# Kernel optimization log

Hardware: AMD Instinct MI355X
Metric: run time of the kernel (lower is better)

Reference implementation:

```python
import jax, jax.numpy as jnp
import numpy as np

TOPN = 1000
MIN_SCORE = 0.05
NMS_THR = 0.5
MAX_OBJ = 100
B, A, C = 8, 100000, 80


def setup_inputs():
    key = jax.random.key(0)
    k1, k2, k3, k4 = jax.random.split(key, 4)
    cls_heads = jax.random.uniform(k1, (B, A, C), dtype=jnp.float32)  # sigmoid-like class scores
    reg_heads = (jax.random.normal(k2, (B, A, 4), dtype=jnp.float32) * 0.1)  # small tx,ty,tw,th
    ctr = jax.random.uniform(k3, (B, A, 2), minval=32.0, maxval=768.0)
    wh = jax.random.uniform(k4, (B, A, 2), minval=16.0, maxval=128.0)
    batch_anchors = jnp.concatenate([ctr - 0.5 * wh, ctr + 0.5 * wh], axis=-1)
    return {"cls_heads": cls_heads, "reg_heads": reg_heads, "batch_anchors": batch_anchors}


def _decode(reg, anchors):
    # snap tx,ty,tw,th to x1y1x2y2; original casts to int (truncation toward zero)
    awh = anchors[..., 2:4] - anchors[..., 0:2]
    actr = anchors[..., 0:2] + 0.5 * awh
    pwh = jnp.exp(reg[..., 2:4]) * awh
    pctr = reg[..., 0:2] * awh + actr
    boxes = jnp.concatenate([pctr - 0.5 * pwh, pctr + 0.5 * pwh], axis=-1)
    return jnp.trunc(boxes)  # matches torch .int() truncation, kept float


def _per_image(scores, classes, boxes):
    # score-threshold filter + descending sort + topn, done as masked top_k (fixed shapes)
    masked = jnp.where(scores > MIN_SCORE, scores, -jnp.inf)
    top_s, idx = jax.lax.top_k(masked, TOPN)
    valid = top_s > MIN_SCORE
    top_c = classes[idx].astype(jnp.float32)
    top_b = boxes[idx]  # [TOPN,4]

    # pairwise IoU (greedy python_nms math)
    wh = top_b[:, 2:4] - top_b[:, 0:2]
    area = jnp.clip(wh[:, 0] * wh[:, 1], 1e-4)  # clamp(min=0.0001)
    tl = jnp.maximum(top_b[:, None, 0:2], top_b[None, :, 0:2])
    br = jnp.minimum(top_b[:, None, 2:4], top_b[None, :, 2:4])
    sz = jnp.clip(br - tl, 0.0)
    inter = sz[..., 0] * sz[..., 1]
    union = jnp.clip(area[:, None] + area[None, :] - inter, 1e-4)
    iou = inter / union  # [TOPN,TOPN]

    ar = jnp.arange(TOPN)

    def body(i, supp):
        # box i, if not already suppressed, suppresses later boxes with iou >= thr
        return supp | ((~supp[i]) & (iou[i] >= NMS_THR) & (ar > i))

    supp = jax.lax.fori_loop(0, TOPN, body, ~valid)
    kept = (~supp) & valid

    # compact first MAX_OBJ kept detections (score order preserved); pad with -1 / zeros
    rank = jnp.cumsum(kept) - 1
    slot = jnp.where(kept & (rank < MAX_OBJ), rank, MAX_OBJ)  # dump slot MAX_OBJ
    out_s = jnp.full((MAX_OBJ + 1,), -1.0, jnp.float32).at[slot].set(jnp.where(kept, top_s, -1.0))[:MAX_OBJ]
    out_c = jnp.full((MAX_OBJ + 1,), -1.0, jnp.float32).at[slot].set(jnp.where(kept, top_c, -1.0))[:MAX_OBJ]
    out_b = jnp.zeros((MAX_OBJ + 1, 4), jnp.float32).at[slot].set(jnp.where(kept[:, None], top_b, 0.0))[:MAX_OBJ]
    return out_s, out_c, out_b


def reference(cls_heads, reg_heads, batch_anchors):
    scores = jnp.max(cls_heads, axis=2)        # [B,A]
    classes = jnp.argmax(cls_heads, axis=2)    # [B,A] int
    boxes = _decode(reg_heads, batch_anchors)  # [B,A,4]
    return jax.vmap(_per_image)(scores, classes, boxes)
```

## Files before the change

kernel.cpp:

```cpp
#include <hip/hip_runtime.h>
#include <cstdint>

#define NB 8
#define NA 100000
#define NC 80
#define TOPN 1000
#define MAXOBJ 100
#define NREG 64
#define REGCAP 256
#define CTRSTRIDE 32
#define SORTN 2048
#define MIN_SCORE 0.05f
#define NMS_THR 0.5f

__global__ __launch_bounds__(256) void k_scores(const float* __restrict__ cls,
                                                unsigned int* __restrict__ keys,
                                                int* __restrict__ clsid,
                                                unsigned long long* __restrict__ cand,
                                                unsigned int* __restrict__ n_cand) {
    const int b = blockIdx.y;
    const int t = threadIdx.x;
    const int lane = t & 63;
    const int sub = lane & 3;
    const int a = blockIdx.x * 64 + (t >> 2);
    const bool valid = (a < NA);
    const int aa = valid ? a : (NA - 1);

    const float4* p = (const float4*)(cls + ((size_t)b * NA + aa) * NC);

    float vm = -1e30f; int vi = 0x7FFFFFFF;
#pragma unroll
    for (int s = 0; s < 5; ++s) {
        float4 v = p[sub + s * 4];
        int c0 = (sub + s * 4) * 4;
        if (v.x > vm) { vm = v.x; vi = c0; }
        if (v.y > vm) { vm = v.y; vi = c0 + 1; }
        if (v.z > vm) { vm = v.z; vi = c0 + 2; }
        if (v.w > vm) { vm = v.w; vi = c0 + 3; }
    }
#pragma unroll
    for (int d = 1; d < 4; d <<= 1) {
        float ovm = __shfl_xor(vm, d);
        int ovi = __shfl_xor(vi, d);
        if (ovm > vm || (ovm == vm && ovi < vi)) { vm = ovm; vi = ovi; }
    }

    unsigned int key = (vm > MIN_SCORE) ? __float_as_uint(vm) : 0u;
    if (valid && sub == 0) {
        size_t o = (size_t)b * NA + a;
        keys[o] = key;
        clsid[o] = vi;
    }

    const unsigned int T0 = __float_as_uint(0.999f);
    bool w = valid && (sub == 0) && (key >= T0);
    unsigned long long m = __ballot(w);
    if (m) {
        const int r = blockIdx.x & (NREG - 1);
        unsigned int* ctr = n_cand + (size_t)((b << 6) | r) * CTRSTRIDE;
        unsigned long long* creg = cand + ((size_t)((b << 6) | r)) * REGCAP;
        int leader = (int)__builtin_ctzll(m);
        unsigned int bs = 0;
        if (lane == leader) bs = atomicAdd(ctr, (unsigned int)__popcll(m));
        bs = __shfl(bs, leader);
        unsigned int pos = bs + (unsigned int)__popcll(m & ((1ull << lane) - 1ull));
        if (w && pos < REGCAP)
            creg[pos] =
                ((unsigned long long)key << 32) |
                (unsigned long long)(0xFFFFFFFFu - (unsigned int)a);
    }
}

__device__ inline void wave_agg_hist(unsigned int* lh, int bin, bool pred) {
    unsigned long long active = __ballot(pred);
    const int lane = threadIdx.x & 63;
    while (active) {
        int leader = (int)__builtin_ctzll(active);
        int lbin = __shfl(bin, leader);
        unsigned long long mask = __ballot(pred && (bin == lbin));
        if (lane == leader) atomicAdd(&lh[lbin], (unsigned int)__popcll(mask));
        active &= ~mask;
    }
}

__device__ inline void top_threshold(const unsigned int* lh, int nbins, int minbin,
                                     unsigned int rank, int* out_bin, unsigned int* out_above) {
    const int lane = threadIdx.x;
    const int chunk = nbins >> 6;
    const int hi = nbins - 1 - lane * chunk;
    const int lo = hi - chunk + 1;
    unsigned int s = 0;
    for (int i = hi; i >= lo; --i)
        if (i >= minbin) s += lh[i];
    unsigned int incl = s;
    for (int d = 1; d < 64; d <<= 1) {
        unsigned int o = __shfl_up(incl, d);
        if (lane >= d) incl += o;
    }
    unsigned int pre = incl - s;
    bool hit = (pre < rank) && (incl >= rank);
    unsigned long long m = __ballot(hit);
    if (m == 0ull) {
        if (lane == 0) { *out_bin = -1; *out_above = 0; }
        return;
    }
    if (hit) {
        unsigned int cum = pre;
        int fb = -1;
        for (int i = hi; i >= lo; --i) {
            if (i < minbin) break;
            unsigned int c = lh[i];
            if (cum + c >= rank) { fb = i; break; }
            cum += c;
        }
        *out_bin = fb;
        *out_above = cum;
    }
}

__global__ __launch_bounds__(1024) void k_select(
    const unsigned int* __restrict__ keys, const int* __restrict__ clsid,
    const unsigned long long* __restrict__ cand, const unsigned int* __restrict__ n_cand,
    const float* __restrict__ reg, const float* __restrict__ anch,
    float* __restrict__ out) {
    __shared__ unsigned int lh[2048];
    __shared__ unsigned long long sk[SORTN];
    __shared__ float4 sbox[TOPN];
    __shared__ float ss[TOPN];
    __shared__ float scl[TOPN];
    __shared__ unsigned int s_rc[NREG];
    __shared__ int s_bin;
    __shared__ unsigned int s_above;
    __shared__ unsigned int s_cnt;
    __shared__ unsigned int s_tot;
    __shared__ int s_ovf;

    const int b = blockIdx.x;
    const int tid = threadIdx.x;
    const int lane = tid & 63;
    const unsigned int* kb = keys + (size_t)b * NA;
    const unsigned long long* cb = cand + ((size_t)b << 6) * REGCAP;
    float* out_s = out + b * MAXOBJ;
    float* out_c = out + NB * MAXOBJ + b * MAXOBJ;
    float* out_b = out + 2 * NB * MAXOBJ + b * MAXOBJ * 4;

    if (tid < MAXOBJ) { out_s[tid] = -1.0f; out_c[tid] = -1.0f; }
    if (tid < MAXOBJ * 4) out_b[tid] = 0.0f;

    if (tid < NREG) {
        unsigned int c = n_cand[(size_t)((b << 6) | tid) * CTRSTRIDE];
        s_rc[tid] = c;
        unsigned int cc = min(c, (unsigned int)REGCAP);
        for (int d = 32; d; d >>= 1) cc += __shfl_down(cc, d);
        unsigned long long om = __ballot(c > REGCAP);
        if (tid == 0) { s_tot = cc; s_ovf = (om != 0ull) ? 1 : 0; }
    }
    __syncthreads();

    const bool fast = (!s_ovf) && (s_tot >= TOPN);
    const int N = fast ? (NREG * REGCAP) : NA;

#define FETCH(i, k, e)                                                        \
    {                                                                         \
        (k) = 0u; (e) = 0ull;                                                 \
        if ((i) < N) {                                                        \
            if (fast) {                                                       \
                int rr = (i) >> 8, pp = (i) & (REGCAP - 1);                   \
                if (pp < (int)s_rc[rr]) {                                     \
                    (e) = cb[i]; (k) = (unsigned int)((e) >> 32);             \
                }                                                             \
            } else {                                                          \
                (k) = kb[i];                                                  \
                (e) = ((unsigned long long)(k) << 32) |                       \
                      (unsigned long long)(0xFFFFFFFFu - (unsigned int)(i));  \
            }                                                                 \
        }                                                                     \
    }

    for (int i = tid; i < 2048; i += 1024) lh[i] = 0;
    __syncthreads();
    for (int base = 0; base < N; base += 1024) {
        int i = base + tid;
        unsigned int k; unsigned long long e;
        FETCH(i, k, e)
        (void)e;
        wave_agg_hist(lh, (int)(k >> 21), k != 0u);
    }
    __syncthreads();
    if (tid < 64) top_threshold(lh, 2048, 1, TOPN, &s_bin, &s_above);
    __syncthreads();
    const int p1 = s_bin;
    const unsigned int above1 = s_above;

    unsigned int T;
    if (p1 < 0) {
        T = 1u;
    } else {
        __syncthreads();
        for (int i = tid; i < 2048; i += 1024) lh[i] = 0;
        __syncthreads();
        for (int base = 0; base < N; base += 1024) {
            int i = base + tid;
            unsigned int k; unsigned long long e;
            FETCH(i, k, e)
            (void)e;
            if (k != 0u && (int)(k >> 21) == p1) atomicAdd(&lh[(k >> 10) & 0x7FFu], 1u);
        }
        __syncthreads();
        if (tid < 64) top_threshold(lh, 2048, 0, TOPN - above1, &s_bin, &s_above);
        __syncthreads();
        const int p2 = s_bin;
        const unsigned int above2 = above1 + s_above;
        if (p2 < 0) {
            T = 1u;
        } else if (above2 + lh[p2] <= SORTN) {
            T = (((unsigned int)p1 << 11) | (unsigned int)p2) << 10;
        } else {
            const unsigned int pref = ((unsigned int)p1 << 11) | (unsigned int)p2;
            __syncthreads();
            for (int i = tid; i < 1024; i += 1024) lh[i] = 0;
            __syncthreads();
            for (int base = 0; base < N; base += 1024) {
                int i = base + tid;
                unsigned int k; unsigned long long e;
                FETCH(i, k, e)
                (void)e;
                if (k != 0u && (k >> 10) == pref) atomicAdd(&lh[k & 0x3FFu], 1u);
            }
            __syncthreads();
            if (tid < 64) top_threshold(lh, 1024, 0, TOPN - above2, &s_bin, &s_above);
            __syncthreads();
            T = (s_bin < 0) ? 1u : ((pref << 10) | (unsigned int)s_bin);
        }
    }
    __syncthreads();

    for (int i = tid; i < SORTN; i += 1024) sk[i] = 0ull;
    if (tid == 0) s_cnt = 0;
    __syncthreads();
    for (int base = 0; base < N; base += 1024) {
        int i = base + tid;
        unsigned int k; unsigned long long e;
        FETCH(i, k, e)
        bool w = (k >= T) && (k != 0u);
        unsigned long long m = __ballot(w);
        if (m) {
            int leader = (int)__builtin_ctzll(m);
            unsigned int bs = 0;
            if (lane == leader) bs = atomicAdd(&s_cnt, (unsigned int)__popcll(m));
            bs = __shfl(bs, leader);
            unsigned int pos = bs + (unsigned int)__popcll(m & ((1ull << lane) - 1ull));
            if (w && pos < SORTN) sk[pos] = e;
        }
    }
    __syncthreads();
#undef FETCH

    for (int k = 2; k <= SORTN; k <<= 1)
        for (int j = k >> 1; j > 0; j >>= 1) {
            __syncthreads();
            for (int i = tid; i < SORTN; i += 1024) {
                int ixj = i ^ j;
                if (ixj > i) {
                    unsigned long long x = sk[i], y = sk[ixj];
                    bool desc = ((i & k) == 0);
                    if (desc ? (x < y) : (x > y)) { sk[i] = y; sk[ixj] = x; }
                }
            }
        }
    __syncthreads();

    if (tid < TOPN) {
        unsigned long long e = sk[tid];
        unsigned int key = (unsigned int)(e >> 32);
        if (key != 0u) {
            int a = (int)(0xFFFFFFFFu - (unsigned int)e);
            size_t base = (size_t)b * NA + a;
            float4 r  = ((const float4*)reg)[base];
            float4 an = ((const float4*)anch)[base];
            float aw = an.z - an.x, ah = an.w - an.y;
            float acx = an.x + 0.5f * aw, acy = an.y + 0.5f * ah;
            float pw = expf(r.z) * aw, ph = expf(r.w) * ah;
            float pcx = r.x * aw + acx, pcy = r.y * ah + acy;
            float4 bx;
            bx.x = truncf(pcx - 0.5f * pw); bx.y = truncf(pcy - 0.5f * ph);
            bx.z = truncf(pcx + 0.5f * pw); bx.w = truncf(pcy + 0.5f * ph);
            sbox[tid] = bx;
            ss[tid] = __uint_as_float(key);
            scl[tid] = (float)clsid[base];
        } else {
            sbox[tid] = make_float4(0.f, 0.f, 0.f, 0.f);
            ss[tid] = -1.0f;
            scl[tid] = -1.0f;
        }
    }
    __syncthreads();
    if (tid >= 64) return;

    float k0x1 = 0, k0y1 = 0, k0x2 = 0, k0y2 = 0, k0a = 0;
    float k1x1 = 0, k1y1 = 0, k1x2 = 0, k1y2 = 0, k1a = 0;
    int kc = 0;
    for (int i = 0; i < TOPN; ++i) {
        float4 bi = sbox[i];
        float si = ss[i];
        if (!(si > MIN_SCORE)) break;
        float areai = fmaxf((bi.z - bi.x) * (bi.w - bi.y), 1e-4f);
        bool sup = false;
        if (lane < kc) {
            float ix = fminf(k0x2, bi.z) - fmaxf(k0x1, bi.x);
            float iy = fminf(k0y2, bi.w) - fmaxf(k0y1, bi.y);
            float inter = fmaxf(ix, 0.0f) * fmaxf(iy, 0.0f);
            float uni = fmaxf(k0a + areai - inter, 1e-4f);
            sup = (inter / uni) >= NMS_THR;
        }
        if (lane + 64 < kc) {
            float ix = fminf(k1x2, bi.z) - fmaxf(k1x1, bi.x);
            float iy = fminf(k1y2, bi.w) - fmaxf(k1y1, bi.y);
            float inter = fmaxf(ix, 0.0f) * fmaxf(iy, 0.0f);
            float uni = fmaxf(k1a + areai - inter, 1e-4f);
            sup = sup || ((inter / uni) >= NMS_THR);
        }
        if (__ballot(sup) == 0ull) {
            if (lane == 0) {
                out_s[kc] = si;
                out_c[kc] = scl[i];
                out_b[kc * 4 + 0] = bi.x; out_b[kc * 4 + 1] = bi.y;
                out_b[kc * 4 + 2] = bi.z; out_b[kc * 4 + 3] = bi.w;
            }
            if (kc < 64) {
                if (lane == kc) { k0x1 = bi.x; k0y1 = bi.y; k0x2 = bi.z; k0y2 = bi.w; k0a = areai; }
            } else {
                if (lane == kc - 64) { k1x1 = bi.x; k1y1 = bi.y; k1x2 = bi.z; k1y2 = bi.w; k1a = areai; }
            }
            ++kc;
            if (kc >= MAXOBJ) break;
        }
    }
}

extern "C" void kernel_launch(void* const* d_in, const int* in_sizes, int n_in,
                              void* d_out, int out_size, void* d_ws, size_t ws_size,
                              hipStream_t stream) {
    const float* cls  = (const float*)d_in[0];
    const float* reg  = (const float*)d_in[1];
    const float* anch = (const float*)d_in[2];
    float* out = (float*)d_out;
    char* ws = (char*)d_ws;

    unsigned int* keys = (unsigned int*)ws;
    int* clsid = (int*)(ws + 3200000);
    unsigned long long* cand = (unsigned long long*)(ws + 6400000);
    unsigned int* n_cand = (unsigned int*)(ws + 7448576);

    hipMemsetAsync(n_cand, 0, (size_t)NB * NREG * CTRSTRIDE * 4, stream);

    dim3 gscore((NA + 63) / 64, NB);
    k_scores<<<gscore, 256, 0, stream>>>(cls, keys, clsid, cand, n_cand);
    k_select<<<NB, 1024, 0, stream>>>(keys, clsid, cand, n_cand, reg, anch, out);
}
```

Baseline: 445.7 us.

## Split NMS into parallel IoU bitmask kernel and serial mask-scan kernel

Splits the fused select kernel into three kernels. The top-k kernel writes sorted boxes, scores and classes to workspace. A grid-wide kernel computes the full pairwise IoU suppression bitmask, and a single-wave kernel per image does the greedy scan using OR-accumulated mask rows. This replaces serial per-candidate IoU against kept boxes with precomputed bitmasks. The cost is computing the full 1000x1000 mask even though scanning stops at 100 kept boxes, plus two extra kernel launches and global-memory round trips.

```diff
diff --git a/kernel.cpp b/kernel.cpp
--- a/kernel.cpp
+++ b/kernel.cpp
@@ -118,16 +118,13 @@
     }
 }
 
-__global__ __launch_bounds__(1024) void k_select(
+__global__ __launch_bounds__(1024) void k_topk(
     const unsigned int* __restrict__ keys, const int* __restrict__ clsid,
     const unsigned long long* __restrict__ cand, const unsigned int* __restrict__ n_cand,
     const float* __restrict__ reg, const float* __restrict__ anch,
-    float* __restrict__ out) {
+    float* __restrict__ sscore, float* __restrict__ sclass, float4* __restrict__ sbox) {
     __shared__ unsigned int lh[2048];
     __shared__ unsigned long long sk[SORTN];
-    __shared__ float4 sbox[TOPN];
-    __shared__ float ss[TOPN];
-    __shared__ float scl[TOPN];
     __shared__ unsigned int s_rc[NREG];
     __shared__ int s_bin;
     __shared__ unsigned int s_above;
@@ -140,12 +137,6 @@
     const int lane = tid & 63;
     const unsigned int* kb = keys + (size_t)b * NA;
     const unsigned long long* cb = cand + ((size_t)b << 6) * REGCAP;
-    float* out_s = out + b * MAXOBJ;
-    float* out_c = out + NB * MAXOBJ + b * MAXOBJ;
-    float* out_b = out + 2 * NB * MAXOBJ + b * MAXOBJ * 4;
-
-    if (tid < MAXOBJ) { out_s[tid] = -1.0f; out_c[tid] = -1.0f; }
-    if (tid < MAXOBJ * 4) out_b[tid] = 0.0f;
 
     if (tid < NREG) {
         unsigned int c = n_cand[(size_t)((b << 6) | tid) * CTRSTRIDE];
@@ -270,6 +261,7 @@
         }
     __syncthreads();
 
+    const size_t wsb = (size_t)b * 1024;
     if (tid < TOPN) {
         unsigned long long e = sk[tid];
         unsigned int key = (unsigned int)(e >> 32);
@@ -285,52 +277,90 @@
             float4 bx;
             bx.x = truncf(pcx - 0.5f * pw); bx.y = truncf(pcy - 0.5f * ph);
             bx.z = truncf(pcx + 0.5f * pw); bx.w = truncf(pcy + 0.5f * ph);
-            sbox[tid] = bx;
-            ss[tid] = __uint_as_float(key);
-            scl[tid] = (float)clsid[base];
+            sbox[wsb + tid] = bx;
+            sscore[wsb + tid] = __uint_as_float(key);
+            sclass[wsb + tid] = (float)clsid[base];
         } else {
-            sbox[tid] = make_float4(0.f, 0.f, 0.f, 0.f);
-            ss[tid] = -1.0f;
-            scl[tid] = -1.0f;
-        }
-    }
-    __syncthreads();
-    if (tid >= 64) return;
-
-    float k0x1 = 0, k0y1 = 0, k0x2 = 0, k0y2 = 0, k0a = 0;
-    float k1x1 = 0, k1y1 = 0, k1x2 = 0, k1y2 = 0, k1a = 0;
+            sbox[wsb + tid] = make_float4(0.f, 0.f, 0.f, 0.f);
+            sscore[wsb + tid] = -1.0f;
+            sclass[wsb + tid] = -1.0f;
+        }
+    } else if (tid < 1024) {
+        sscore[wsb + tid] = -1.0f;
+    }
+}
+
+__global__ __launch_bounds__(256) void k_nmsmask(
+    const float* __restrict__ sscore, const float4* __restrict__ sbox,
+    unsigned long long* __restrict__ masks) {
+    const int b = blockIdx.y;
+    const int lane = threadIdx.x & 63;
+    const int i = blockIdx.x * 4 + (threadIdx.x >> 6);
+    if (i >= TOPN) return;
+    const size_t wsb = (size_t)b * 1024;
+    if (!(sscore[wsb + i] > MIN_SCORE)) return;
+
+    const float4 bi = sbox[wsb + i];
+    const float ai = fmaxf((bi.z - bi.x) * (bi.w - bi.y), 1e-4f);
+    unsigned long long* mrow = masks + ((size_t)b * 1024 + i) * 16;
+
+#pragma unroll 4
+    for (int c = 0; c < 16; ++c) {
+        int j = c * 64 + lane;
+        float4 bj = sbox[wsb + j];
+        float aj = fmaxf((bj.z - bj.x) * (bj.w - bj.y), 1e-4f);
+        float ix = fminf(bi.z, bj.z) - fmaxf(bi.x, bj.x);
+        float iy = fminf(bi.w, bj.w) - fmaxf(bi.y, bj.y);
+        float inter = fmaxf(ix, 0.0f) * fmaxf(iy, 0.0f);
+        float uni = fmaxf(ai + aj - inter, 1e-4f);
+        bool pred = (j > i) && (j < TOPN) && (inter / uni >= NMS_THR);
+        unsigned long long m = __ballot(pred);
+        if (lane == 0) mrow[c] = m;
+    }
+}
+
+__global__ __launch_bounds__(64) void k_nmsout(
+    const float* __restrict__ sscore, const float* __restrict__ sclass,
+    const float4* __restrict__ sbox, const unsigned long long* __restrict__ masks,
+    float* __restrict__ out) {
+    const int b = blockIdx.x;
+    const int lane = threadIdx.x;
+    float* out_s = out + b * MAXOBJ;
+    float* out_c = out + NB * MAXOBJ + b * MAXOBJ;
+    float* out_b = out + 2 * NB * MAXOBJ + b * MAXOBJ * 4;
+
+    for (int i = lane; i < MAXOBJ; i += 64) { out_s[i] = -1.0f; out_c[i] = -1.0f; }
+    for (int i = lane; i < MAXOBJ * 4; i += 64) out_b[i] = 0.0f;
+
+    const size_t wsb = (size_t)b * 1024;
+    const float* ssb = sscore + wsb;
+    const float* scb = sclass + wsb;
+    const float4* sbb = sbox + wsb;
+    const unsigned long long* mb = masks + wsb * 16;
+
+    unsigned long long vbits = 0ull;
+    for (int c = 0; c < 16; ++c) {
+        unsigned long long m = __ballot(ssb[c * 64 + lane] > MIN_SCORE);
+        if (lane == c) vbits = m;
+    }
+
+    unsigned long long acc = 0ull;
     int kc = 0;
     for (int i = 0; i < TOPN; ++i) {
-        float4 bi = sbox[i];
-        float si = ss[i];
-        if (!(si > MIN_SCORE)) break;
-        float areai = fmaxf((bi.z - bi.x) * (bi.w - bi.y), 1e-4f);
-        bool sup = false;
-        if (lane < kc) {
-            float ix = fminf(k0x2, bi.z) - fmaxf(k0x1, bi.x);
-            float iy = fminf(k0y2, bi.w) - fmaxf(k0y1, bi.y);
-            float inter = fmaxf(ix, 0.0f) * fmaxf(iy, 0.0f);
-            float uni = fmaxf(k0a + areai - inter, 1e-4f);
-            sup = (inter / uni) >= NMS_THR;
-        }
-        if (lane + 64 < kc) {
-            float ix = fminf(k1x2, bi.z) - fmaxf(k1x1, bi.x);
-            float iy = fminf(k1y2, bi.w) - fmaxf(k1y1, bi.y);
-            float inter = fmaxf(ix, 0.0f) * fmaxf(iy, 0.0f);
-            float uni = fmaxf(k1a + areai - inter, 1e-4f);
-            sup = sup || ((inter / uni) >= NMS_THR);
-        }
-        if (__ballot(sup) == 0ull) {
+        const int chunk = i >> 6;
+        const unsigned long long bit = 1ull << (i & 63);
+        const bool mine = (lane == chunk);
+        if (__ballot(mine && ((vbits & bit) == 0ull)))
+            break;
+        bool sup = (__ballot(mine && ((acc & bit) != 0ull)) != 0ull);
+        if (!sup) {
+            if (lane < 16) acc |= mb[(size_t)i * 16 + lane];
             if (lane == 0) {
-                out_s[kc] = si;
-                out_c[kc] = scl[i];
-                out_b[kc * 4 + 0] = bi.x; out_b[kc * 4 + 1] = bi.y;
-                out_b[kc * 4 + 2] = bi.z; out_b[kc * 4 + 3] = bi.w;
-            }
-            if (kc < 64) {
-                if (lane == kc) { k0x1 = bi.x; k0y1 = bi.y; k0x2 = bi.z; k0y2 = bi.w; k0a = areai; }
-            } else {
-                if (lane == kc - 64) { k1x1 = bi.x; k1y1 = bi.y; k1x2 = bi.z; k1y2 = bi.w; k1a = areai; }
+                out_s[kc] = ssb[i];
+                out_c[kc] = scb[i];
+                float4 bx = sbb[i];
+                out_b[kc * 4 + 0] = bx.x; out_b[kc * 4 + 1] = bx.y;
+                out_b[kc * 4 + 2] = bx.z; out_b[kc * 4 + 3] = bx.w;
             }
             ++kc;
             if (kc >= MAXOBJ) break;
@@ -351,10 +381,18 @@
     int* clsid = (int*)(ws + 3200000);
     unsigned long long* cand = (unsigned long long*)(ws + 6400000);
     unsigned int* n_cand = (unsigned int*)(ws + 7448576);
+    float4* sbox = (float4*)(ws + 7514112);
+    float* sscore = (float*)(ws + 7645184);
+    float* sclass = (float*)(ws + 7677952);
+    unsigned long long* masks = (unsigned long long*)(ws + 7710720);
 
     hipMemsetAsync(n_cand, 0, (size_t)NB * NREG * CTRSTRIDE * 4, stream);
 
     dim3 gscore((NA + 63) / 64, NB);
     k_scores<<<gscore, 256, 0, stream>>>(cls, keys, clsid, cand, n_cand);
-    k_select<<<NB, 1024, 0, stream>>>(keys, clsid, cand, n_cand, reg, anch, out);
-}
+    k_topk<<<NB, 1024, 0, stream>>>(keys, clsid, cand, n_cand, reg, anch,
+                                    sscore, sclass, sbox);
+    dim3 gmask((TOPN + 3) / 4, NB);
+    k_nmsmask<<<gmask, 256, 0, stream>>>(sscore, sbox, masks);
+    k_nmsout<<<NB, 64, 0, stream>>>(sscore, sclass, sbox, masks, out);
+}
```

Result: slower. 480.4 us (+7.8%).
